# Kernel tuning notes

Measured on AMD Instinct MI355X. Metric: run time of the kernel, lower is better.

The kernel has to match this reference:

```python
import jax, jax.numpy as jnp
import numpy as np

B = 16384
D = 4096  # d_mlp == d_hidden in this module
K = 64


def setup_inputs() -> dict:
    key = jax.random.key(0)
    k1, k2, k3, k4 = jax.random.split(key, 4)
    x = jax.random.normal(k1, (B, D), dtype=jnp.float32)
    ema_frequency_counter = jax.random.uniform(k2, (D,), dtype=jnp.float32)
    W_enc = jax.random.normal(k3, (D, D), dtype=jnp.float32)
    # W_dec initialized like the module: randn, then scaled by 0.1/(norm+2*eps-ish);
    # the exact init scaling: norm over dim=1, norm += eps(=1), then *= 0.1/(norm+eps)
    W_dec_raw = jax.random.normal(k4, (D, D), dtype=jnp.float32)
    eps = 1.0
    norm = jnp.linalg.norm(W_dec_raw, axis=1, keepdims=True) + eps
    W_dec = W_dec_raw * (0.1 / (norm + eps))
    pre_bias = jnp.zeros((D,), dtype=jnp.float32)
    latent_bias = jnp.zeros((D,), dtype=jnp.float32)
    return {
        'x': x,
        'ema_frequency_counter': ema_frequency_counter,
        'W_enc': W_enc,
        'W_dec': W_dec,
        'pre_bias': pre_bias,
        'latent_bias': latent_bias,
        'k': K,
    }


def topk_activation(acts, k):
    # torch.topk -> ReLU on values -> scatter back into zeros
    vals, idx = jax.lax.top_k(acts, k)          # [B, k]
    vals = jax.nn.relu(vals)
    rows = jnp.arange(acts.shape[0])[:, None]   # [B, 1]
    return jnp.zeros_like(acts).at[rows, idx].set(vals)


def reference(x, ema_frequency_counter, W_enc, W_dec, pre_bias, latent_bias, k):
    # method='reconstruct' path of TopKAutoEncoder.forward
    x_center = x - pre_bias                     # [B, D]
    acts = x_center @ W_enc + latent_bias       # [B, D]
    acts_top_k = topk_activation(acts, k)       # sparse (k nonzeros/row)
    x_reconstruct = acts_top_k @ W_dec + pre_bias
    return x_reconstruct
```

## Files before the change

### kernel.cpp

```cpp
#include <hip/hip_runtime.h>
#include <hip/hip_bf16.h>
#include <stdint.h>


typedef _Float16 half8 __attribute__((ext_vector_type(8)));
typedef float f32x4 __attribute__((ext_vector_type(4)));
typedef unsigned short ushort8 __attribute__((ext_vector_type(8)));

#define B_ROWS 16384
#define D_DIM  4096
#define TOPK   64
#define EBOUND 0.3f
#define NTILES (D_DIM / 32)

__device__ __forceinline__ void gload_lds16(const void* g, void* l) {
  __builtin_amdgcn_global_load_lds(
      (const __attribute__((address_space(1))) unsigned int*)g,
      (__attribute__((address_space(3))) unsigned int*)l, 16, 0, 0);
}

__device__ __forceinline__ unsigned f32_sortable(float f) {
  unsigned u = __float_as_uint(f);
  return (u & 0x80000000u) ? ~u : (u | 0x80000000u);
}
__device__ __forceinline__ float sortable_f32(unsigned u) {
  return __uint_as_float((u & 0x80000000u) ? (u & 0x7fffffffu) : ~u);
}
__device__ __forceinline__ unsigned short f2bf(float f) {
  unsigned u = __float_as_uint(f);
  unsigned r = (u + 0x7fffu + ((u >> 16) & 1u)) >> 16;
  return (unsigned short)r;
}


__global__ __launch_bounds__(256) void conv_x(
    const float* __restrict__ x, const float* __restrict__ pre_bias,
    _Float16* __restrict__ Xh) {
  size_t g = ((size_t)blockIdx.x * 256 + threadIdx.x) * 8;
  int col = (int)(g & (D_DIM - 1));
  float4 a = *(const float4*)(x + g);
  float4 b = *(const float4*)(x + g + 4);
  float4 p = *(const float4*)(pre_bias + col);
  float4 q = *(const float4*)(pre_bias + col + 4);
  half8 h;
  h[0] = (_Float16)(a.x - p.x); h[1] = (_Float16)(a.y - p.y);
  h[2] = (_Float16)(a.z - p.z); h[3] = (_Float16)(a.w - p.w);
  h[4] = (_Float16)(b.x - q.x); h[5] = (_Float16)(b.y - q.y);
  h[6] = (_Float16)(b.z - q.z); h[7] = (_Float16)(b.w - q.w);
  *(half8*)(Xh + g) = h;
}

__global__ __launch_bounds__(256) void transp_w(
    const float* __restrict__ W, _Float16* __restrict__ WhT,
    float* __restrict__ WT) {
  __shared__ float tile[64][65];
  int bx = blockIdx.x, by = blockIdx.y;
  int tx = threadIdx.x & 63, ty4 = threadIdx.x >> 6;
  #pragma unroll 4
  for (int i = 0; i < 16; ++i) {
    int r = ty4 * 16 + i;
    tile[r][tx] = W[(size_t)(by * 64 + r) * D_DIM + bx * 64 + tx];
  }
  __syncthreads();
  #pragma unroll 4
  for (int i = 0; i < 16; ++i) {
    int r = ty4 * 16 + i;
    float v = tile[tx][r];
    size_t o = (size_t)(bx * 64 + r) * D_DIM + by * 64 + tx;
    WT[o] = v;
    WhT[o] = (_Float16)v;
  }
}

__global__ __launch_bounds__(256) void conv_wd(
    const float* __restrict__ W, unsigned short* __restrict__ o) {
  size_t g = ((size_t)blockIdx.x * 256 + threadIdx.x) * 8;
  float4 a = *(const float4*)(W + g);
  float4 b = *(const float4*)(W + g + 4);
  ushort8 v;
  v[0] = f2bf(a.x); v[1] = f2bf(a.y); v[2] = f2bf(a.z); v[3] = f2bf(a.w);
  v[4] = f2bf(b.x); v[5] = f2bf(b.y); v[6] = f2bf(b.z); v[7] = f2bf(b.w);
  *(ushort8*)(o + g) = v;
}


#define TILE_BODY(T, VMSTR)                                                    \
  do {                                                                         \
    asm volatile("s_waitcnt " VMSTR ::: "memory");                             \
    __builtin_amdgcn_s_barrier();                                              \
    asm volatile("" ::: "memory");                                             \
    const int tt3 = (T) + 3;                                                   \
    if (tt3 < NTILES) {                                                        \
      const int bo = (tt3 & 3) * 8192;                                         \
      const int kk = tt3 * 32;                                                 \
      gload_lds16(aSrc0 + kk, AsB + bo + dst0);                                \
      gload_lds16(aSrc1 + kk, AsB + bo + dst1);                                \
    }                                                                          \
    {                                                                          \
      const int ab = ((T) & 3) * 8192;                                         \
      half8 bf[4], af[4];                                                      \
      _Pragma("unroll") for (int nj = 0; nj < 4; ++nj)                         \
          bf[nj] = *(const half8*)(BsB + ab + bBase + nj * 512);               \
      _Pragma("unroll") for (int mi = 0; mi < 4; ++mi)                         \
          af[mi] = *(const half8*)(AsB + ab + aBase + mi * 512);               \
      __builtin_amdgcn_s_setprio(1);                                           \
      _Pragma("unroll") for (int mi = 0; mi < 4; ++mi)                         \
          _Pragma("unroll") for (int nj = 0; nj < 4; ++nj)                     \
          acc[mi][nj] = __builtin_amdgcn_mfma_f32_16x16x32_f16(                \
              af[mi], bf[nj], acc[mi][nj], 0, 0, 0);                           \
      __builtin_amdgcn_s_setprio(0);                                           \
      if (tt3 < NTILES) {                                                      \
        const int bo = (tt3 & 3) * 8192;                                       \
        const int kk = tt3 * 32;                                               \
        gload_lds16(bSrc0 + kk, BsB + bo + dst0);                              \
        gload_lds16(bSrc1 + kk, BsB + bo + dst1);                              \
      }                                                                        \
      _Pragma("unroll") for (int mi = 0; mi < 4; ++mi)                         \
          af[mi] = *(const half8*)(AsB + ab + aBase + (mi + 4) * 512);         \
      __builtin_amdgcn_s_setprio(1);                                           \
      _Pragma("unroll") for (int mi = 0; mi < 4; ++mi)                         \
          _Pragma("unroll") for (int nj = 0; nj < 4; ++nj)                     \
          acc[mi + 4][nj] = __builtin_amdgcn_mfma_f32_16x16x32_f16(            \
              af[mi], bf[nj], acc[mi + 4][nj], 0, 0, 0);                       \
      __builtin_amdgcn_s_setprio(0);                                           \
    }                                                                          \
  } while (0)

__global__ __launch_bounds__(512, 2) void gemm_f16(
    const _Float16* __restrict__ A, const _Float16* __restrict__ Bt,
    const float* __restrict__ latent_bias, float* __restrict__ C) {
  extern __shared__ _Float16 ldsbuf[];
  _Float16* AsB = ldsbuf;
  _Float16* BsB = ldsbuf + 4 * 8192;

  const int tid = threadIdx.x;
  const int lane = tid & 63, wave = tid >> 6;
  const int wr = wave >> 2, wc = wave & 3;

  int bid = blockIdx.x;
  int swz = (bid & 7) * (1024 >> 3) + (bid >> 3);
  const int bmBase = (swz >> 4) * 256;
  const int bnBase = (swz & 15) * 256;

  const int i0 = tid, i1 = 512 + tid;
  const int s0 = i0 ^ ((i0 >> 3) & 3), s1 = i1 ^ ((i1 >> 3) & 3);
  const _Float16* aSrc0 = A + (size_t)(bmBase + (s0 >> 2)) * D_DIM + (s0 & 3) * 8;
  const _Float16* aSrc1 = A + (size_t)(bmBase + (s1 >> 2)) * D_DIM + (s1 & 3) * 8;
  const _Float16* bSrc0 = Bt + (size_t)(bnBase + (s0 >> 2)) * D_DIM + (s0 & 3) * 8;
  const _Float16* bSrc1 = Bt + (size_t)(bnBase + (s1 >> 2)) * D_DIM + (s1 & 3) * 8;
  const int dst0 = i0 * 8, dst1 = i1 * 8;

  const int fr = lane & 15, c4 = lane >> 4;
  const int swzc = (c4 ^ ((fr >> 1) & 3)) * 8;
  const int aBase = (wr * 128 + fr) * 32 + swzc;
  const int bBase = (wc * 64 + fr) * 32 + swzc;

  f32x4 acc[8][4];
  #pragma unroll
  for (int i = 0; i < 8; ++i)
    #pragma unroll
    for (int j = 0; j < 4; ++j) acc[i][j] = f32x4{0.f, 0.f, 0.f, 0.f};

  #pragma unroll
  for (int tt = 0; tt < 3; ++tt) {
    const int bo = tt * 8192, kk = tt * 32;
    gload_lds16(aSrc0 + kk, AsB + bo + dst0);
    gload_lds16(aSrc1 + kk, AsB + bo + dst1);
    gload_lds16(bSrc0 + kk, BsB + bo + dst0);
    gload_lds16(bSrc1 + kk, BsB + bo + dst1);
  }

  for (int t = 0; t < NTILES - 2; ++t) TILE_BODY(t, "vmcnt(8)");
  TILE_BODY(NTILES - 2, "vmcnt(4)");
  TILE_BODY(NTILES - 1, "vmcnt(0)");

  const int crow0 = bmBase + wr * 128 + c4 * 4;
  const int ccol0 = bnBase + wc * 64 + fr;
  #pragma unroll
  for (int mi = 0; mi < 8; ++mi)
    #pragma unroll
    for (int nj = 0; nj < 4; ++nj) {
      int col = ccol0 + nj * 16;
      float lb = latent_bias[col];
      #pragma unroll
      for (int r = 0; r < 4; ++r)
        C[(size_t)(crow0 + mi * 16 + r) * D_DIM + col] = acc[mi][nj][r] + lb;
    }
}


__global__ __launch_bounds__(256) void topk_classify(
    const float* __restrict__ acts, float* __restrict__ vals,
    int* __restrict__ idxs, int* __restrict__ ambIdx,
    int* __restrict__ rowMeta) {
  const int row = blockIdx.x;
  const int tid = threadIdx.x;
  const int lane = tid & 63, wave = tid >> 6;
  __shared__ int sred[4];
  const float* arow = acts + (size_t)row * D_DIM;
  unsigned su[16];
  #pragma unroll
  for (int i = 0; i < 4; ++i) {
    float4 a = *(const float4*)(arow + i * 1024 + tid * 4);
    su[4 * i + 0] = f32_sortable(a.x);
    su[4 * i + 1] = f32_sortable(a.y);
    su[4 * i + 2] = f32_sortable(a.z);
    su[4 * i + 3] = f32_sortable(a.w);
  }
  unsigned thr = 0u;
  for (int b = 31; b >= 12; --b) {
    unsigned cand = thr | (1u << b);
    int c = 0;
    #pragma unroll
    for (int i = 0; i < 16; ++i) c += (su[i] >= cand) ? 1 : 0;
    #pragma unroll
    for (int off = 32; off; off >>= 1) c += __shfl_down(c, off);
    if (lane == 0) sred[wave] = c;
    __syncthreads();
    int tot = sred[0] + sred[1] + sred[2] + sred[3];
    if (tot >= TOPK) thr = cand;
    __syncthreads();
  }
  float Tlo = sortable_f32(thr);
  float Thi = sortable_f32(thr + 4096u);
  unsigned uhi = f32_sortable(Thi + 2.0f * EBOUND);
  unsigned ulo = f32_sortable(Tlo - 2.0f * EBOUND);
  int mC = 0, aC = 0;
  #pragma unroll
  for (int i = 0; i < 16; ++i) {
    unsigned u = su[i];
    if (u > uhi) ++mC;
    else if (u >= ulo) ++aC;
  }
  int xs = mC | (aC << 16);
  #pragma unroll
  for (int off = 1; off < 64; off <<= 1) {
    int y = __shfl_up(xs, off);
    if (lane >= off) xs += y;
  }
  if (lane == 63) sred[wave] = xs;
  __syncthreads();
  int base = 0;
  for (int w = 0; w < 4; ++w)
    if (w < wave) base += sred[w];
  int tot = sred[0] + sred[1] + sred[2] + sred[3];
  int incl = base + xs;
  int mp = (incl & 0xffff) - mC;
  int ap = (incl >> 16) - aC;
  int mTot = tot & 0xffff, aTot = tot >> 16;
  #pragma unroll
  for (int e = 0; e < 16; ++e) {
    unsigned u = su[e];
    int d = (e >> 2) * 1024 + tid * 4 + (e & 3);
    if (u > uhi) {
      vals[(size_t)row * TOPK + mp] = fmaxf(sortable_f32(u), 0.0f);
      idxs[(size_t)row * TOPK + mp] = d;
      ++mp;
    } else if (u >= ulo) {
      if (ap < 128) ambIdx[(size_t)row * 128 + ap] = d;
      ++ap;
    }
  }
  if (tid == 0) {
    rowMeta[row * 2 + 0] = mTot;
    rowMeta[row * 2 + 1] = (aTot > 128) ? 128 : aTot;
  }
}


__global__ __launch_bounds__(256) void rescue(
    const float* __restrict__ x, const float* __restrict__ WT,
    const float* __restrict__ pre_bias, const float* __restrict__ latent_bias,
    const float* __restrict__ acts, const int* __restrict__ ambIdx,
    const int* __restrict__ rowMeta, float* __restrict__ vals,
    int* __restrict__ idxs) {
  const int row = blockIdx.x;
  const int m = rowMeta[row * 2 + 0];
  const int s = rowMeta[row * 2 + 1];
  const int need = TOPK - m;
  const int tid = threadIdx.x;
  if (need <= 0 || s <= 0) return;
  if (s == need) {
    if (tid < s) {
      int d = ambIdx[(size_t)row * 128 + tid];
      float v = acts[(size_t)row * D_DIM + d];
      vals[(size_t)row * TOPK + m + tid] = fmaxf(v, 0.0f);
      idxs[(size_t)row * TOPK + m + tid] = d;
    }
    return;
  }
  __shared__ double exv[128];
  const int lane = tid & 63, wave = tid >> 6;
  const float* xr = x + (size_t)row * D_DIM;
  for (int c = wave; c < s; c += 4) {
    int d = ambIdx[(size_t)row * 128 + c];
    const float* wrow = WT + (size_t)d * D_DIM;
    double acc = 0.0;
    #pragma unroll 4
    for (int t = 0; t < 16; ++t) {
      int k0 = t * 256 + lane * 4;
      float4 xv = *(const float4*)(xr + k0);
      float4 pv = *(const float4*)(pre_bias + k0);
      float4 wv = *(const float4*)(wrow + k0);
      acc = fma((double)xv.x - (double)pv.x, (double)wv.x, acc);
      acc = fma((double)xv.y - (double)pv.y, (double)wv.y, acc);
      acc = fma((double)xv.z - (double)pv.z, (double)wv.z, acc);
      acc = fma((double)xv.w - (double)pv.w, (double)wv.w, acc);
    }
    #pragma unroll
    for (int off = 32; off; off >>= 1) acc += __shfl_down(acc, off);
    if (lane == 0) exv[c] = acc + (double)latent_bias[d];
  }
  __syncthreads();
  if (tid == 0) {
    for (int t = 0; t < need; ++t) {
      double best = -1.0e300; int besti = 1 << 30; int bestc = -1;
      for (int c = 0; c < s; ++c) {
        double v = exv[c];
        int d = ambIdx[(size_t)row * 128 + c];
        if (v > best || (v == best && d < besti)) {
          best = v; besti = d; bestc = c;
        }
      }
      vals[(size_t)row * TOPK + m + t] = fmaxf((float)best, 0.0f);
      idxs[(size_t)row * TOPK + m + t] = besti;
      exv[bestc] = -1.0e300;
    }
  }
}


__global__ __launch_bounds__(256) void reconstruct(
    const unsigned short* __restrict__ Wd, const float* __restrict__ vals,
    const int* __restrict__ idxs, const float* __restrict__ pre_bias,
    float* __restrict__ out) {
  const int bid = blockIdx.x;
  const int cb = bid & 7, rowblk = bid >> 3;
  const int tid = threadIdx.x, lane = tid & 63, wave = tid >> 6;
  const int row = rowblk * 4 + wave;
  const int col0 = cb * 512 + lane * 8;
  __shared__ float sval[256];
  __shared__ int sidx[256];
  sval[tid] = vals[(size_t)(rowblk * 4 + (tid >> 6)) * TOPK + (tid & 63)];
  sidx[tid] = idxs[(size_t)(rowblk * 4 + (tid >> 6)) * TOPK + (tid & 63)];
  __syncthreads();
  float acc[8];
  float4 p0 = *(const float4*)(pre_bias + col0);
  float4 p1 = *(const float4*)(pre_bias + col0 + 4);
  acc[0] = p0.x; acc[1] = p0.y; acc[2] = p0.z; acc[3] = p0.w;
  acc[4] = p1.x; acc[5] = p1.y; acc[6] = p1.z; acc[7] = p1.w;
  #pragma unroll 4
  for (int k = 0; k < TOPK; ++k) {
    float v = sval[wave * 64 + k];
    int d = sidx[wave * 64 + k];
    ushort8 w = *(const ushort8*)(Wd + (size_t)d * D_DIM + col0);
    #pragma unroll
    for (int j = 0; j < 8; ++j)
      acc[j] = fmaf(v, __uint_as_float(((unsigned)w[j]) << 16), acc[j]);
  }
  float4 o0 = {acc[0], acc[1], acc[2], acc[3]};
  float4 o1 = {acc[4], acc[5], acc[6], acc[7]};
  *(float4*)(out + (size_t)row * D_DIM + col0) = o0;
  *(float4*)(out + (size_t)row * D_DIM + col0 + 4) = o1;
}


extern "C" void kernel_launch(void* const* d_in, const int* in_sizes, int n_in,
                              void* d_out, int out_size, void* d_ws,
                              size_t ws_size, hipStream_t stream) {
  const float* x           = (const float*)d_in[0];
  const float* W_enc       = (const float*)d_in[2];
  const float* W_dec       = (const float*)d_in[3];
  const float* pre_bias    = (const float*)d_in[4];
  const float* latent_bias = (const float*)d_in[5];
  float* out = (float*)d_out;
  char* ws = (char*)d_ws;
  size_t off = 0;
  auto alloc = [&](size_t bytes) {
    size_t o = off;
    off = (off + bytes + 255) & ~(size_t)255;
    return o;
  };
  _Float16* Xh        = (_Float16*)(ws + alloc((size_t)B_ROWS * D_DIM * 2));
  _Float16* WhT       = (_Float16*)(ws + alloc((size_t)D_DIM * D_DIM * 2));
  float* WT           = (float*)(ws + alloc((size_t)D_DIM * D_DIM * 4));
  unsigned short* Wd  = (unsigned short*)(ws + alloc((size_t)D_DIM * D_DIM * 2));
  float* vals         = (float*)(ws + alloc((size_t)B_ROWS * TOPK * 4));
  int* idxs           = (int*)(ws + alloc((size_t)B_ROWS * TOPK * 4));
  int* ambIdx         = (int*)(ws + alloc((size_t)B_ROWS * 128 * 4));
  int* rowMeta        = (int*)(ws + alloc((size_t)B_ROWS * 2 * 4));
  (void)ws_size; (void)in_sizes; (void)n_in; (void)out_size;

  (void)hipFuncSetAttribute((const void*)gemm_f16,
                            hipFuncAttributeMaxDynamicSharedMemorySize,
                            131072);

  conv_x<<<(B_ROWS * D_DIM / 8) / 256, 256, 0, stream>>>(x, pre_bias, Xh);
  transp_w<<<dim3(D_DIM / 64, D_DIM / 64), 256, 0, stream>>>(W_enc, WhT, WT);
  conv_wd<<<((size_t)D_DIM * D_DIM / 8) / 256, 256, 0, stream>>>(W_dec, Wd);
  gemm_f16<<<(B_ROWS / 256) * (D_DIM / 256), 512, 131072, stream>>>(
      Xh, WhT, latent_bias, out);
  topk_classify<<<B_ROWS, 256, 0, stream>>>(out, vals, idxs, ambIdx, rowMeta);
  rescue<<<B_ROWS, 256, 0, stream>>>(x, WT, pre_bias, latent_bias, out,
                                     ambIdx, rowMeta, vals, idxs);
  reconstruct<<<(B_ROWS / 4) * 8, 256, 0, stream>>>(Wd, vals, idxs, pre_bias,
                                                    out);
}
```

Measured before the change: 1.285 ms.

## Double-buffer GEMM register fragments and narrow top-k ambiguity margin with fast path

The f16 GEMM main loop now issues all four global-to-LDS loads for tile t+3 together and prefetches the next tile's A/B fragments from LDS into alternating register sets while the current MFMAs run, so LDS read latency is hidden. The top-k classifier shrinks the ambiguity band around the threshold from 0.6 to 0.25. When the ambiguous count exactly fills the remaining slots, it writes those candidates directly and skips the rescue pass. A narrower margin assumes the f16 GEMM error stays below it, which risks picking a different top-k set, and the extra register buffers raise register pressure at 2 waves/SIMD.

```diff
diff --git a/kernel.cpp b/kernel.cpp
--- a/kernel.cpp
+++ b/kernel.cpp
@@ -10,7 +10,7 @@
 #define B_ROWS 16384
 #define D_DIM  4096
 #define TOPK   64
-#define EBOUND 0.3f
+#define MARGIN 0.25f
 #define NTILES (D_DIM / 32)
 
 __device__ __forceinline__ void gload_lds16(const void* g, void* l) {
@@ -84,44 +84,48 @@
 }
 
 
-#define TILE_BODY(T, VMSTR)                                                    \
+#define STAGE(T)                                                               \
+  do {                                                                         \
+    const int bo_ = ((T) & 3) * 8192;                                          \
+    const int kk_ = (T) * 32;                                                  \
+    gload_lds16(aSrc0 + kk_, AsB + bo_ + dst0);                                \
+    gload_lds16(aSrc1 + kk_, AsB + bo_ + dst1);                                \
+    gload_lds16(bSrc0 + kk_, BsB + bo_ + dst0);                                \
+    gload_lds16(bSrc1 + kk_, BsB + bo_ + dst1);                                \
+  } while (0)
+
+#define PREFETCH(T, AF, BF)                                                    \
+  do {                                                                         \
+    const int ab_ = ((T) & 3) * 8192;                                          \
+    _Pragma("unroll") for (int nj = 0; nj < 4; ++nj)                           \
+        BF[nj] = *(const half8*)(BsB + ab_ + bBase + nj * 512);                \
+    _Pragma("unroll") for (int mi = 0; mi < 4; ++mi)                           \
+        AF[mi] = *(const half8*)(AsB + ab_ + aBase + mi * 512);                \
+  } while (0)
+
+#define BODY(T, AFC, BFC, AFN, BFN, VMSTR)                                     \
   do {                                                                         \
     asm volatile("s_waitcnt " VMSTR ::: "memory");                             \
     __builtin_amdgcn_s_barrier();                                              \
     asm volatile("" ::: "memory");                                             \
-    const int tt3 = (T) + 3;                                                   \
-    if (tt3 < NTILES) {                                                        \
-      const int bo = (tt3 & 3) * 8192;                                         \
-      const int kk = tt3 * 32;                                                 \
-      gload_lds16(aSrc0 + kk, AsB + bo + dst0);                                \
-      gload_lds16(aSrc1 + kk, AsB + bo + dst1);                                \
-    }                                                                          \
+    if ((T) + 3 < NTILES) STAGE((T) + 3);                                      \
+    if ((T) + 1 < NTILES) PREFETCH((T) + 1, AFN, BFN);                         \
+    __builtin_amdgcn_s_setprio(1);                                             \
+    _Pragma("unroll") for (int mi = 0; mi < 4; ++mi)                           \
+        _Pragma("unroll") for (int nj = 0; nj < 4; ++nj)                       \
+        acc[mi][nj] = __builtin_amdgcn_mfma_f32_16x16x32_f16(                  \
+            AFC[mi], BFC[nj], acc[mi][nj], 0, 0, 0);                           \
+    __builtin_amdgcn_s_setprio(0);                                             \
     {                                                                          \
-      const int ab = ((T) & 3) * 8192;                                         \
-      half8 bf[4], af[4];                                                      \
-      _Pragma("unroll") for (int nj = 0; nj < 4; ++nj)                         \
-          bf[nj] = *(const half8*)(BsB + ab + bBase + nj * 512);               \
+      const int ab_ = ((T) & 3) * 8192;                                        \
+      half8 af2[4];                                                            \
       _Pragma("unroll") for (int mi = 0; mi < 4; ++mi)                         \
-          af[mi] = *(const half8*)(AsB + ab + aBase + mi * 512);               \
-      __builtin_amdgcn_s_setprio(1);                                           \
-      _Pragma("unroll") for (int mi = 0; mi < 4; ++mi)                         \
-          _Pragma("unroll") for (int nj = 0; nj < 4; ++nj)                     \
-          acc[mi][nj] = __builtin_amdgcn_mfma_f32_16x16x32_f16(                \
-              af[mi], bf[nj], acc[mi][nj], 0, 0, 0);                           \
-      __builtin_amdgcn_s_setprio(0);                                           \
-      if (tt3 < NTILES) {                                                      \
-        const int bo = (tt3 & 3) * 8192;                                       \
-        const int kk = tt3 * 32;                                               \
-        gload_lds16(bSrc0 + kk, BsB + bo + dst0);                              \
-        gload_lds16(bSrc1 + kk, BsB + bo + dst1);                              \
-      }                                                                        \
-      _Pragma("unroll") for (int mi = 0; mi < 4; ++mi)                         \
-          af[mi] = *(const half8*)(AsB + ab + aBase + (mi + 4) * 512);         \
+          af2[mi] = *(const half8*)(AsB + ab_ + aBase + (mi + 4) * 512);       \
       __builtin_amdgcn_s_setprio(1);                                           \
       _Pragma("unroll") for (int mi = 0; mi < 4; ++mi)                         \
           _Pragma("unroll") for (int nj = 0; nj < 4; ++nj)                     \
           acc[mi + 4][nj] = __builtin_amdgcn_mfma_f32_16x16x32_f16(            \
-              af[mi], bf[nj], acc[mi + 4][nj], 0, 0, 0);                       \
+              af2[mi], BFC[nj], acc[mi + 4][nj], 0, 0, 0);                     \
       __builtin_amdgcn_s_setprio(0);                                           \
     }                                                                          \
   } while (0)
@@ -161,18 +165,19 @@
     #pragma unroll
     for (int j = 0; j < 4; ++j) acc[i][j] = f32x4{0.f, 0.f, 0.f, 0.f};
 
-  #pragma unroll
-  for (int tt = 0; tt < 3; ++tt) {
-    const int bo = tt * 8192, kk = tt * 32;
-    gload_lds16(aSrc0 + kk, AsB + bo + dst0);
-    gload_lds16(aSrc1 + kk, AsB + bo + dst1);
-    gload_lds16(bSrc0 + kk, BsB + bo + dst0);
-    gload_lds16(bSrc1 + kk, BsB + bo + dst1);
-  }
-
-  for (int t = 0; t < NTILES - 2; ++t) TILE_BODY(t, "vmcnt(8)");
-  TILE_BODY(NTILES - 2, "vmcnt(4)");
-  TILE_BODY(NTILES - 1, "vmcnt(0)");
+  STAGE(0); STAGE(1); STAGE(2);
+  asm volatile("s_waitcnt vmcnt(8)" ::: "memory");
+  __builtin_amdgcn_s_barrier();
+  asm volatile("" ::: "memory");
+  half8 afA[4], bfA[4], afB[4], bfB[4];
+  PREFETCH(0, afA, bfA);
+
+  for (int t = 0; t < NTILES - 2; t += 2) {
+    BODY(t, afA, bfA, afB, bfB, "vmcnt(4)");
+    BODY(t + 1, afB, bfB, afA, bfA, "vmcnt(4)");
+  }
+  BODY(NTILES - 2, afA, bfA, afB, bfB, "vmcnt(0)");
+  BODY(NTILES - 1, afB, bfB, afA, bfA, "vmcnt(0)");
 
   const int crow0 = bmBase + wr * 128 + c4 * 4;
   const int ccol0 = bnBase + wc * 64 + fr;
@@ -223,8 +228,8 @@
   }
   float Tlo = sortable_f32(thr);
   float Thi = sortable_f32(thr + 4096u);
-  unsigned uhi = f32_sortable(Thi + 2.0f * EBOUND);
-  unsigned ulo = f32_sortable(Tlo - 2.0f * EBOUND);
+  unsigned uhi = f32_sortable(Thi + MARGIN);
+  unsigned ulo = f32_sortable(Tlo - MARGIN);
   int mC = 0, aC = 0;
   #pragma unroll
   for (int i = 0; i < 16; ++i) {
@@ -248,6 +253,8 @@
   int mp = (incl & 0xffff) - mC;
   int ap = (incl >> 16) - aC;
   int mTot = tot & 0xffff, aTot = tot >> 16;
+  const int need = TOPK - mTot;
+  const bool fast = (aTot == need);
   #pragma unroll
   for (int e = 0; e < 16; ++e) {
     unsigned u = su[e];
@@ -257,13 +264,18 @@
       idxs[(size_t)row * TOPK + mp] = d;
       ++mp;
     } else if (u >= ulo) {
-      if (ap < 128) ambIdx[(size_t)row * 128 + ap] = d;
+      if (fast) {
+        vals[(size_t)row * TOPK + mTot + ap] = fmaxf(sortable_f32(u), 0.0f);
+        idxs[(size_t)row * TOPK + mTot + ap] = d;
+      } else if (ap < 128) {
+        ambIdx[(size_t)row * 128 + ap] = d;
+      }
       ++ap;
     }
   }
   if (tid == 0) {
     rowMeta[row * 2 + 0] = mTot;
-    rowMeta[row * 2 + 1] = (aTot > 128) ? 128 : aTot;
+    rowMeta[row * 2 + 1] = (fast || need <= 0) ? 0 : ((aTot > 128) ? 128 : aTot);
   }
 }
 
```

Result: faster. 1.209 ms (-5.9%).

## Replace bitwise radix threshold search with LDS histogram and fast ambiguous path

Applied to the files above, without the earlier changes.

The top-k classifier no longer finds its threshold with a 20-step bitwise radix search, which needed two block barriers per step. It now builds a 4096-bin shared-memory histogram over a fixed value range, takes a suffix scan, and picks the threshold bin in one pass. When the number of ambiguous candidates exactly fills the remaining top-k slots, they are written straight to the output and the row skips the rescue kernel. The trade-offs are shared-memory atomic contention, a bin range fixed to the expected activation scale, and a slightly narrower safety margin around the threshold. The GEMM tile macro is redefined with the same body.

```diff
diff --git a/kernel.cpp b/kernel.cpp
--- a/kernel.cpp
+++ b/kernel.cpp
@@ -10,7 +10,7 @@
 #define B_ROWS 16384
 #define D_DIM  4096
 #define TOPK   64
-#define EBOUND 0.3f
+#define MARGIN 0.25f
 #define NTILES (D_DIM / 32)
 
 __device__ __forceinline__ void gload_lds16(const void* g, void* l) {
@@ -19,13 +19,6 @@
       (__attribute__((address_space(3))) unsigned int*)l, 16, 0, 0);
 }
 
-__device__ __forceinline__ unsigned f32_sortable(float f) {
-  unsigned u = __float_as_uint(f);
-  return (u & 0x80000000u) ? ~u : (u | 0x80000000u);
-}
-__device__ __forceinline__ float sortable_f32(unsigned u) {
-  return __uint_as_float((u & 0x80000000u) ? (u & 0x7fffffffu) : ~u);
-}
 __device__ __forceinline__ unsigned short f2bf(float f) {
   unsigned u = __float_as_uint(f);
   unsigned r = (u + 0x7fffu + ((u >> 16) & 1u)) >> 16;
@@ -121,6 +114,49 @@
       _Pragma("unroll") for (int mi = 0; mi < 4; ++mi)                         \
           _Pragma("unroll") for (int nj = 0; nj < 4; ++nj)                     \
           acc[mi + 4][nj] = __builtin_amdgcn_mfma_f32_16x16x32_f16(            \
+              af2[mi], bf[nj], acc[mi + 4][nj], 0, 0, 0);                      \
+      __builtin_amdgcn_s_setprio(0);                                           \
+    }                                                                          \
+  } while (0)
+
+#undef TILE_BODY
+#define TILE_BODY(T, VMSTR)                                                    \
+  do {                                                                         \
+    asm volatile("s_waitcnt " VMSTR ::: "memory");                             \
+    __builtin_amdgcn_s_barrier();                                              \
+    asm volatile("" ::: "memory");                                             \
+    const int tt3 = (T) + 3;                                                   \
+    if (tt3 < NTILES) {                                                        \
+      const int bo = (tt3 & 3) * 8192;                                         \
+      const int kk = tt3 * 32;                                                 \
+      gload_lds16(aSrc0 + kk, AsB + bo + dst0);                                \
+      gload_lds16(aSrc1 + kk, AsB + bo + dst1);                                \
+    }                                                                          \
+    {                                                                          \
+      const int ab = ((T) & 3) * 8192;                                         \
+      half8 bf[4], af[4];                                                      \
+      _Pragma("unroll") for (int nj = 0; nj < 4; ++nj)                         \
+          bf[nj] = *(const half8*)(BsB + ab + bBase + nj * 512);               \
+      _Pragma("unroll") for (int mi = 0; mi < 4; ++mi)                         \
+          af[mi] = *(const half8*)(AsB + ab + aBase + mi * 512);               \
+      __builtin_amdgcn_s_setprio(1);                                           \
+      _Pragma("unroll") for (int mi = 0; mi < 4; ++mi)                         \
+          _Pragma("unroll") for (int nj = 0; nj < 4; ++nj)                     \
+          acc[mi][nj] = __builtin_amdgcn_mfma_f32_16x16x32_f16(                \
+              af[mi], bf[nj], acc[mi][nj], 0, 0, 0);                           \
+      __builtin_amdgcn_s_setprio(0);                                           \
+      if (tt3 < NTILES) {                                                      \
+        const int bo = (tt3 & 3) * 8192;                                       \
+        const int kk = tt3 * 32;                                               \
+        gload_lds16(bSrc0 + kk, BsB + bo + dst0);                              \
+        gload_lds16(bSrc1 + kk, BsB + bo + dst1);                              \
+      }                                                                        \
+      _Pragma("unroll") for (int mi = 0; mi < 4; ++mi)                         \
+          af[mi] = *(const half8*)(AsB + ab + aBase + (mi + 4) * 512);         \
+      __builtin_amdgcn_s_setprio(1);                                           \
+      _Pragma("unroll") for (int mi = 0; mi < 4; ++mi)                         \
+          _Pragma("unroll") for (int nj = 0; nj < 4; ++nj)                     \
+          acc[mi + 4][nj] = __builtin_amdgcn_mfma_f32_16x16x32_f16(            \
               af[mi], bf[nj], acc[mi + 4][nj], 0, 0, 0);                       \
       __builtin_amdgcn_s_setprio(0);                                           \
     }                                                                          \
@@ -196,41 +232,65 @@
   const int row = blockIdx.x;
   const int tid = threadIdx.x;
   const int lane = tid & 63, wave = tid >> 6;
-  __shared__ int sred[4];
+  __shared__ int hist[4096];
+  __shared__ int sred[8];
   const float* arow = acts + (size_t)row * D_DIM;
-  unsigned su[16];
+  float fv[16];
   #pragma unroll
   for (int i = 0; i < 4; ++i) {
     float4 a = *(const float4*)(arow + i * 1024 + tid * 4);
-    su[4 * i + 0] = f32_sortable(a.x);
-    su[4 * i + 1] = f32_sortable(a.y);
-    su[4 * i + 2] = f32_sortable(a.z);
-    su[4 * i + 3] = f32_sortable(a.w);
-  }
-  unsigned thr = 0u;
-  for (int b = 31; b >= 12; --b) {
-    unsigned cand = thr | (1u << b);
-    int c = 0;
-    #pragma unroll
-    for (int i = 0; i < 16; ++i) c += (su[i] >= cand) ? 1 : 0;
-    #pragma unroll
-    for (int off = 32; off; off >>= 1) c += __shfl_down(c, off);
-    if (lane == 0) sred[wave] = c;
-    __syncthreads();
-    int tot = sred[0] + sred[1] + sred[2] + sred[3];
-    if (tot >= TOPK) thr = cand;
-    __syncthreads();
-  }
-  float Tlo = sortable_f32(thr);
-  float Thi = sortable_f32(thr + 4096u);
-  unsigned uhi = f32_sortable(Thi + 2.0f * EBOUND);
-  unsigned ulo = f32_sortable(Tlo - 2.0f * EBOUND);
+    fv[4 * i + 0] = a.x; fv[4 * i + 1] = a.y;
+    fv[4 * i + 2] = a.z; fv[4 * i + 3] = a.w;
+  }
+  #pragma unroll
+  for (int i = 0; i < 16; ++i) hist[tid * 16 + i] = 0;
+  __syncthreads();
+  #pragma unroll
+  for (int e = 0; e < 16; ++e) {
+    int b = (int)((fv[e] + 512.0f) * 4.0f);
+    b = b < 0 ? 0 : (b > 4095 ? 4095 : b);
+    atomicAdd(&hist[b], 1);
+  }
+  __syncthreads();
+  int loc[16];
+  int s = 0;
+  #pragma unroll
+  for (int i = 15; i >= 0; --i) { s += hist[tid * 16 + i]; loc[i] = s; }
+  int x = s;
+  #pragma unroll
+  for (int off = 1; off < 64; off <<= 1) {
+    int y = __shfl_down(x, off);
+    if (lane + off < 64) x += y;
+  }
+  if (lane == 0) sred[wave] = x;
+  __syncthreads();
+  int after = 0;
+  for (int w = wave + 1; w < 4; ++w) after += sred[w];
+  const int sufAfter = (x - s) + after;
+  int cand = -1;
+  #pragma unroll
+  for (int i = 0; i < 16; ++i)
+    if (loc[i] + sufAfter >= TOPK) cand = tid * 16 + i;
+  #pragma unroll
+  for (int off = 32; off; off >>= 1) {
+    int y = __shfl_down(cand, off);
+    cand = y > cand ? y : cand;
+  }
+  if (lane == 0) sred[4 + wave] = cand;
+  __syncthreads();
+  int b0 = sred[4] > sred[5] ? sred[4] : sred[5];
+  int b1 = sred[6] > sred[7] ? sred[6] : sred[7];
+  const int bstar = b0 > b1 ? b0 : b1;
+  const float Tlo = (bstar == 0) ? -1e30f : (bstar * 0.25f - 512.0f);
+  const float Thi = (bstar >= 4095) ? 1e30f : ((bstar + 1) * 0.25f - 512.0f);
+  const float vhi = Thi + MARGIN;
+  const float vlo = Tlo - MARGIN;
   int mC = 0, aC = 0;
   #pragma unroll
   for (int i = 0; i < 16; ++i) {
-    unsigned u = su[i];
-    if (u > uhi) ++mC;
-    else if (u >= ulo) ++aC;
+    float v = fv[i];
+    if (v > vhi) ++mC;
+    else if (v >= vlo) ++aC;
   }
   int xs = mC | (aC << 16);
   #pragma unroll
@@ -248,22 +308,29 @@
   int mp = (incl & 0xffff) - mC;
   int ap = (incl >> 16) - aC;
   int mTot = tot & 0xffff, aTot = tot >> 16;
+  const int need = TOPK - mTot;
+  const bool fast = (aTot == need);
   #pragma unroll
   for (int e = 0; e < 16; ++e) {
-    unsigned u = su[e];
+    float v = fv[e];
     int d = (e >> 2) * 1024 + tid * 4 + (e & 3);
-    if (u > uhi) {
-      vals[(size_t)row * TOPK + mp] = fmaxf(sortable_f32(u), 0.0f);
+    if (v > vhi) {
+      vals[(size_t)row * TOPK + mp] = fmaxf(v, 0.0f);
       idxs[(size_t)row * TOPK + mp] = d;
       ++mp;
-    } else if (u >= ulo) {
-      if (ap < 128) ambIdx[(size_t)row * 128 + ap] = d;
+    } else if (v >= vlo) {
+      if (fast) {
+        vals[(size_t)row * TOPK + mTot + ap] = fmaxf(v, 0.0f);
+        idxs[(size_t)row * TOPK + mTot + ap] = d;
+      } else if (ap < 128) {
+        ambIdx[(size_t)row * 128 + ap] = d;
+      }
       ++ap;
     }
   }
   if (tid == 0) {
     rowMeta[row * 2 + 0] = mTot;
-    rowMeta[row * 2 + 1] = (aTot > 128) ? 128 : aTot;
+    rowMeta[row * 2 + 1] = (fast || need <= 0) ? 0 : ((aTot > 128) ? 128 : aTot);
   }
 }
 
```

Result: faster. 1.158 ms (-9.9%).
